# Performance work log

Measured on AMD Instinct MI355X. Metric: run time of the kernel, lower is better.

Reference implementation:

```python
import jax, jax.numpy as jnp
import numpy as np

N_TERMS = 2048  # zonotope error terms (x[0] center + 2047 generators)
N = 4096        # neurons


def setup_inputs() -> dict:
    key = jax.random.key(0)
    x = jax.random.normal(key, (N_TERMS, N), dtype=jnp.float32)
    return {"x": x}


def reference(x):
    n_terms, n = x.shape
    # interval bounds of the zonotope
    abs_sum = jnp.sum(jnp.abs(x[1:]), axis=0)      # [n]
    upper = x[0] + abs_sum
    lower = x[0] - abs_sum

    cross = (lower * upper) < 0                    # neuron straddles 0
    pos = lower >= 0                               # strictly non-negative
    crossf = cross.astype(x.dtype)
    posf = pos.astype(x.dtype)

    # 'auto' lambda init: upper/(upper-lower) on crossing neurons, 1 on positive,
    # NaN (0/0) replaced by 0.5; lambda is set via .data => constant w.r.t. x.
    denom = upper - lower
    safe = denom != 0
    lam = posf + crossf * jnp.where(safe, upper / jnp.where(safe, denom, 1.0), 0.5)
    lam = jax.lax.stop_gradient(lam)

    delta = jnp.maximum(-lam * lower, (1.0 - lam) * upper)  # [n]

    center = (delta * 0.5 + lam * x[0]) * crossf + x[0] * posf
    gens = x[1:] * (lam * crossf + posf)                    # [n_terms-1, n]

    # Parallel stream-compaction: crossing neuron i gets its own new error row
    # at n_terms + (# crossings before i). Padded to worst case n new rows;
    # non-crossing writes land on distinct (row, col) slots with value 0.
    ci = cross.astype(jnp.int32)
    rows = n_terms + jnp.cumsum(ci) - ci               # exclusive prefix sum
    cols = jnp.arange(n)

    out = jnp.zeros((n_terms + n, n), x.dtype)
    out = out.at[0].set(center)
    out = out.at[1:n_terms].set(gens)
    out = out.at[rows, cols].add((delta * 0.5) * crossf)
    return out
```

## Files before the change

kernel.cpp:

```cpp
#include <hip/hip_runtime.h>

#define N_TERMS 2048
#define NCOL 4096
#define NC4 1024
#define NCHUNK 128
#define RPC (N_TERMS / NCHUNK)

typedef float f4_t __attribute__((ext_vector_type(4)));

__global__ void k_pass1(const float* __restrict__ x, float* __restrict__ partial,
                        float* __restrict__ out, int* __restrict__ done_ctr) {
    const int b = blockIdx.x;
    const int t = threadIdx.x;
    if (b < 512) {
        if (b == 0 && t == 0) *done_ctr = 0;
        const int col4 = (b & 3) * 256 + t;
        const int chunk = b >> 2;
        int r0 = chunk * RPC;
        const int r1 = r0 + RPC;
        if (r0 == 0) r0 = 1;
        const f4_t* x4 = (const f4_t*)x;
        f4_t acc = {0.f, 0.f, 0.f, 0.f};
#pragma unroll
        for (int r = r0; r < r1; ++r) {
            f4_t v = x4[(long)r * NC4 + col4];
            acc.x += fabsf(v.x);
            acc.y += fabsf(v.y);
            acc.z += fabsf(v.z);
            acc.w += fabsf(v.w);
        }
        ((f4_t*)partial)[chunk * NC4 + col4] = acc;
    } else {
        const int zb = b - 512;
        f4_t* o4 = (f4_t*)out;
        const long base4 = (long)N_TERMS * NC4 + (long)zb * 2048;
        const f4_t z = {0.f, 0.f, 0.f, 0.f};
#pragma unroll
        for (int i = 0; i < 8; ++i)
            __builtin_nontemporal_store(z, &o4[base4 + i * 256 + t]);
    }
}

__global__ void k_stats(const float* __restrict__ x, const float* __restrict__ partial,
                        float* __restrict__ out, float* __restrict__ scale,
                        float* __restrict__ dhalf, int* __restrict__ crossflag,
                        int* __restrict__ done_ctr) {
    const int t = threadIdx.x;
    const int lane = t & 63;
    const int q = t >> 6;
    const int c = blockIdx.x * 64 + lane;

    float s0 = 0.f, s1 = 0.f, s2 = 0.f, s3 = 0.f;
    const int k0 = q * 32;
#pragma unroll 8
    for (int k = 0; k < 32; k += 4) {
        s0 += partial[(k0 + k + 0) * NCOL + c];
        s1 += partial[(k0 + k + 1) * NCOL + c];
        s2 += partial[(k0 + k + 2) * NCOL + c];
        s3 += partial[(k0 + k + 3) * NCOL + c];
    }
    __shared__ float red[4][64];
    red[q][lane] = (s0 + s1) + (s2 + s3);
    __syncthreads();
    if (q == 0) {
        float s = (red[0][lane] + red[1][lane]) + (red[2][lane] + red[3][lane]);
        float x0 = x[c];
        float u = x0 + s;
        float l = x0 - s;
        bool cross = (l * u) < 0.0f;
        bool pos = (l >= 0.0f);
        float denom = u - l;
        float lam = (pos ? 1.0f : 0.0f) +
                    (cross ? ((denom != 0.0f) ? u / denom : 0.5f) : 0.0f);
        float delta = fmaxf(-lam * l, (1.0f - lam) * u);
        float crossf = cross ? 1.0f : 0.0f;
        float posf = pos ? 1.0f : 0.0f;
        out[c] = (delta * 0.5f + lam * x0) * crossf + x0 * posf;
        scale[c] = lam * crossf + posf;
        dhalf[c] = delta * 0.5f * crossf;
        crossflag[c] = cross ? 1 : 0;
    }

    __threadfence();
    __shared__ int is_last;
    if (t == 0) is_last = (atomicAdd(done_ctr, 1) == (int)gridDim.x - 1);
    __syncthreads();
    if (!is_last) return;
    __threadfence();

    const int T = 256;
    const int PER = NCOL / T;
    __shared__ int tsum[T];
    const int base = t * PER;
    int cf[PER];
    int ex[PER];
    int run = 0;
#pragma unroll
    for (int i = 0; i < PER; ++i) {
        cf[i] = crossflag[base + i];
        ex[i] = run;
        run += cf[i];
    }
    tsum[t] = run;
    __syncthreads();
    for (int off = 1; off < T; off <<= 1) {
        int v = 0;
        if (t >= off) v = tsum[t - off];
        __syncthreads();
        tsum[t] += v;
        __syncthreads();
    }
    const int excl = (t == 0) ? 0 : tsum[t - 1];
#pragma unroll
    for (int i = 0; i < PER; ++i) {
        if (cf[i]) {
            const int c2 = base + i;
            const long row = N_TERMS + excl + ex[i];
            out[row * (long)NCOL + c2] = dhalf[c2];
        }
    }
}

__global__ void k_gens(const float* __restrict__ x, const float* __restrict__ scale,
                       float* __restrict__ out) {
    const int g = blockIdx.x * blockDim.x + threadIdx.x;
    const int col4 = g & 1023;
    const int group = g >> 10;
    const int r0 = group << 2;
    const f4_t* x4 = (const f4_t*)x;
    f4_t* o4 = (f4_t*)out;
    const f4_t sc = ((const f4_t*)scale)[col4];

    if (group == 0) {
#pragma unroll
        for (int r = 1; r < 4; ++r) {
            f4_t v = x4[(long)r * NC4 + col4] * sc;
            __builtin_nontemporal_store(v, &o4[(long)r * NC4 + col4]);
        }
    } else {
#pragma unroll
        for (int i = 0; i < 4; ++i) {
            const int r = r0 + i;
            f4_t v = x4[(long)r * NC4 + col4] * sc;
            __builtin_nontemporal_store(v, &o4[(long)r * NC4 + col4]);
        }
    }
}

extern "C" void kernel_launch(void* const* d_in, const int* in_sizes, int n_in,
                              void* d_out, int out_size, void* d_ws, size_t ws_size,
                              hipStream_t stream) {
    const float* x = (const float*)d_in[0];
    float* out = (float*)d_out;

    float* ws = (float*)d_ws;
    float* partial   = ws;
    float* scale     = partial + NCHUNK * NCOL;
    float* dhalf     = scale + NCOL;
    int*   crossflag = (int*)(dhalf + NCOL);
    int*   done_ctr  = crossflag + NCOL;

    k_pass1<<<2560, 256, 0, stream>>>(x, partial, out, done_ctr);
    k_stats<<<64, 256, 0, stream>>>(x, partial, out, scale, dhalf, crossflag, done_ctr);
    k_gens<<<2048, 256, 0, stream>>>(x, scale, out);
}
```

Measured before the change: 146.5 us.

## Reassign zero-fill and scan across kernels, drop last-block atomic handoff

Moves the zeroing of the padded tail rows from the abs-sum pass into the stats kernel, which now runs 512 extra blocks that each write four times as much, so the zero-fill overlaps the small stats computation. The prefix-scan scatter is taken out of the stats kernel's last-block atomic/threadfence pattern and becomes one extra block in the generator-scaling kernel. This removes the done counter and its fences. The cost is that the serial scan block now runs alongside the large gens kernel instead of alone.

```diff
diff --git a/kernel.cpp b/kernel.cpp
--- a/kernel.cpp
+++ b/kernel.cpp
@@ -8,141 +8,137 @@
 
 typedef float f4_t __attribute__((ext_vector_type(4)));
 
-__global__ void k_pass1(const float* __restrict__ x, float* __restrict__ partial,
-                        float* __restrict__ out, int* __restrict__ done_ctr) {
+__global__ void k_partial_abs(const float* __restrict__ x, float* __restrict__ partial) {
+    int col4 = blockIdx.x * blockDim.x + threadIdx.x;
+    int chunk = blockIdx.y;
+    int r0 = chunk * RPC;
+    int r1 = r0 + RPC;
+    if (r0 == 0) r0 = 1;
+    const f4_t* x4 = (const f4_t*)x;
+    f4_t acc = {0.f, 0.f, 0.f, 0.f};
+#pragma unroll
+    for (int r = r0; r < r1; ++r) {
+        f4_t v = x4[(long)r * NC4 + col4];
+        acc.x += fabsf(v.x);
+        acc.y += fabsf(v.y);
+        acc.z += fabsf(v.z);
+        acc.w += fabsf(v.w);
+    }
+    ((f4_t*)partial)[chunk * NC4 + col4] = acc;
+}
+
+__global__ void k_stats_zero(const float* __restrict__ x, const float* __restrict__ partial,
+                             float* __restrict__ out, float* __restrict__ scale,
+                             float* __restrict__ dhalf, int* __restrict__ crossflag) {
     const int b = blockIdx.x;
     const int t = threadIdx.x;
-    if (b < 512) {
-        if (b == 0 && t == 0) *done_ctr = 0;
-        const int col4 = (b & 3) * 256 + t;
-        const int chunk = b >> 2;
-        int r0 = chunk * RPC;
-        const int r1 = r0 + RPC;
-        if (r0 == 0) r0 = 1;
-        const f4_t* x4 = (const f4_t*)x;
-        f4_t acc = {0.f, 0.f, 0.f, 0.f};
-#pragma unroll
-        for (int r = r0; r < r1; ++r) {
-            f4_t v = x4[(long)r * NC4 + col4];
-            acc.x += fabsf(v.x);
-            acc.y += fabsf(v.y);
-            acc.z += fabsf(v.z);
-            acc.w += fabsf(v.w);
+
+    if (b < 64) {
+        const int lane = t & 63;
+        const int q = t >> 6;
+        const int c = b * 64 + lane;
+
+        float s0 = 0.f, s1 = 0.f, s2 = 0.f, s3 = 0.f;
+        const int k0 = q * 32;
+#pragma unroll 8
+        for (int k = 0; k < 32; k += 4) {
+            s0 += partial[(k0 + k + 0) * NCOL + c];
+            s1 += partial[(k0 + k + 1) * NCOL + c];
+            s2 += partial[(k0 + k + 2) * NCOL + c];
+            s3 += partial[(k0 + k + 3) * NCOL + c];
         }
-        ((f4_t*)partial)[chunk * NC4 + col4] = acc;
+        __shared__ float red[4][64];
+        red[q][lane] = (s0 + s1) + (s2 + s3);
+        __syncthreads();
+        if (q == 0) {
+            float s = (red[0][lane] + red[1][lane]) + (red[2][lane] + red[3][lane]);
+            float x0 = x[c];
+            float u = x0 + s;
+            float l = x0 - s;
+            bool cross = (l * u) < 0.0f;
+            bool pos = (l >= 0.0f);
+            float denom = u - l;
+            float lam = (pos ? 1.0f : 0.0f) +
+                        (cross ? ((denom != 0.0f) ? u / denom : 0.5f) : 0.0f);
+            float delta = fmaxf(-lam * l, (1.0f - lam) * u);
+            float crossf = cross ? 1.0f : 0.0f;
+            float posf = pos ? 1.0f : 0.0f;
+            out[c] = (delta * 0.5f + lam * x0) * crossf + x0 * posf;
+            scale[c] = lam * crossf + posf;
+            dhalf[c] = delta * 0.5f * crossf;
+            crossflag[c] = cross ? 1 : 0;
+        }
     } else {
-        const int zb = b - 512;
+        const int zb = b - 64;
         f4_t* o4 = (f4_t*)out;
-        const long base4 = (long)N_TERMS * NC4 + (long)zb * 2048;
+        const long base4 = (long)N_TERMS * NC4 + (long)zb * 8192;
         const f4_t z = {0.f, 0.f, 0.f, 0.f};
 #pragma unroll
-        for (int i = 0; i < 8; ++i)
+        for (int i = 0; i < 32; ++i)
             __builtin_nontemporal_store(z, &o4[base4 + i * 256 + t]);
     }
 }
 
-__global__ void k_stats(const float* __restrict__ x, const float* __restrict__ partial,
-                        float* __restrict__ out, float* __restrict__ scale,
-                        float* __restrict__ dhalf, int* __restrict__ crossflag,
-                        int* __restrict__ done_ctr) {
+__global__ void k_gens_scatter(const float* __restrict__ x, const float* __restrict__ scale,
+                               const float* __restrict__ dhalf,
+                               const int* __restrict__ crossflag,
+                               float* __restrict__ out) {
+    const int b = blockIdx.x;
     const int t = threadIdx.x;
-    const int lane = t & 63;
-    const int q = t >> 6;
-    const int c = blockIdx.x * 64 + lane;
+    if (b < 2048) {
+        const int g = b * 256 + t;
+        const int col4 = g & 1023;
+        const int group = g >> 10;
+        const int r0 = group << 2;
+        const f4_t* x4 = (const f4_t*)x;
+        f4_t* o4 = (f4_t*)out;
+        const f4_t sc = ((const f4_t*)scale)[col4];
 
-    float s0 = 0.f, s1 = 0.f, s2 = 0.f, s3 = 0.f;
-    const int k0 = q * 32;
-#pragma unroll 8
-    for (int k = 0; k < 32; k += 4) {
-        s0 += partial[(k0 + k + 0) * NCOL + c];
-        s1 += partial[(k0 + k + 1) * NCOL + c];
-        s2 += partial[(k0 + k + 2) * NCOL + c];
-        s3 += partial[(k0 + k + 3) * NCOL + c];
-    }
-    __shared__ float red[4][64];
-    red[q][lane] = (s0 + s1) + (s2 + s3);
-    __syncthreads();
-    if (q == 0) {
-        float s = (red[0][lane] + red[1][lane]) + (red[2][lane] + red[3][lane]);
-        float x0 = x[c];
-        float u = x0 + s;
-        float l = x0 - s;
-        bool cross = (l * u) < 0.0f;
-        bool pos = (l >= 0.0f);
-        float denom = u - l;
-        float lam = (pos ? 1.0f : 0.0f) +
-                    (cross ? ((denom != 0.0f) ? u / denom : 0.5f) : 0.0f);
-        float delta = fmaxf(-lam * l, (1.0f - lam) * u);
-        float crossf = cross ? 1.0f : 0.0f;
-        float posf = pos ? 1.0f : 0.0f;
-        out[c] = (delta * 0.5f + lam * x0) * crossf + x0 * posf;
-        scale[c] = lam * crossf + posf;
-        dhalf[c] = delta * 0.5f * crossf;
-        crossflag[c] = cross ? 1 : 0;
-    }
-
-    __threadfence();
-    __shared__ int is_last;
-    if (t == 0) is_last = (atomicAdd(done_ctr, 1) == (int)gridDim.x - 1);
-    __syncthreads();
-    if (!is_last) return;
-    __threadfence();
-
-    const int T = 256;
-    const int PER = NCOL / T;
-    __shared__ int tsum[T];
-    const int base = t * PER;
-    int cf[PER];
-    int ex[PER];
-    int run = 0;
+        if (group == 0) {
 #pragma unroll
-    for (int i = 0; i < PER; ++i) {
-        cf[i] = crossflag[base + i];
-        ex[i] = run;
-        run += cf[i];
-    }
-    tsum[t] = run;
-    __syncthreads();
-    for (int off = 1; off < T; off <<= 1) {
-        int v = 0;
-        if (t >= off) v = tsum[t - off];
-        __syncthreads();
-        tsum[t] += v;
-        __syncthreads();
-    }
-    const int excl = (t == 0) ? 0 : tsum[t - 1];
+            for (int r = 1; r < 4; ++r) {
+                f4_t v = x4[(long)r * NC4 + col4] * sc;
+                __builtin_nontemporal_store(v, &o4[(long)r * NC4 + col4]);
+            }
+        } else {
 #pragma unroll
-    for (int i = 0; i < PER; ++i) {
-        if (cf[i]) {
-            const int c2 = base + i;
-            const long row = N_TERMS + excl + ex[i];
-            out[row * (long)NCOL + c2] = dhalf[c2];
-        }
-    }
-}
-
-__global__ void k_gens(const float* __restrict__ x, const float* __restrict__ scale,
-                       float* __restrict__ out) {
-    const int g = blockIdx.x * blockDim.x + threadIdx.x;
-    const int col4 = g & 1023;
-    const int group = g >> 10;
-    const int r0 = group << 2;
-    const f4_t* x4 = (const f4_t*)x;
-    f4_t* o4 = (f4_t*)out;
-    const f4_t sc = ((const f4_t*)scale)[col4];
-
-    if (group == 0) {
-#pragma unroll
-        for (int r = 1; r < 4; ++r) {
-            f4_t v = x4[(long)r * NC4 + col4] * sc;
-            __builtin_nontemporal_store(v, &o4[(long)r * NC4 + col4]);
+            for (int i = 0; i < 4; ++i) {
+                const int r = r0 + i;
+                f4_t v = x4[(long)r * NC4 + col4] * sc;
+                __builtin_nontemporal_store(v, &o4[(long)r * NC4 + col4]);
+            }
         }
     } else {
+        const int T = 256;
+        const int PER = NCOL / T;
+        __shared__ int tsum[T];
+        const int base = t * PER;
+        int cf[PER];
+        int ex[PER];
+        int run = 0;
 #pragma unroll
-        for (int i = 0; i < 4; ++i) {
-            const int r = r0 + i;
-            f4_t v = x4[(long)r * NC4 + col4] * sc;
-            __builtin_nontemporal_store(v, &o4[(long)r * NC4 + col4]);
+        for (int i = 0; i < PER; ++i) {
+            cf[i] = crossflag[base + i];
+            ex[i] = run;
+            run += cf[i];
+        }
+        tsum[t] = run;
+        __syncthreads();
+        for (int off = 1; off < T; off <<= 1) {
+            int v = 0;
+            if (t >= off) v = tsum[t - off];
+            __syncthreads();
+            tsum[t] += v;
+            __syncthreads();
+        }
+        const int excl = (t == 0) ? 0 : tsum[t - 1];
+#pragma unroll
+        for (int i = 0; i < PER; ++i) {
+            if (cf[i]) {
+                const int c = base + i;
+                const long row = N_TERMS + excl + ex[i];
+                out[row * (long)NCOL + c] = dhalf[c];
+            }
         }
     }
 }
@@ -158,9 +154,8 @@
     float* scale     = partial + NCHUNK * NCOL;
     float* dhalf     = scale + NCOL;
     int*   crossflag = (int*)(dhalf + NCOL);
-    int*   done_ctr  = crossflag + NCOL;
 
-    k_pass1<<<2560, 256, 0, stream>>>(x, partial, out, done_ctr);
-    k_stats<<<64, 256, 0, stream>>>(x, partial, out, scale, dhalf, crossflag, done_ctr);
-    k_gens<<<2048, 256, 0, stream>>>(x, scale, out);
+    k_partial_abs<<<dim3(NC4 / 256, NCHUNK), 256, 0, stream>>>(x, partial);
+    k_stats_zero<<<576, 256, 0, stream>>>(x, partial, out, scale, dhalf, crossflag);
+    k_gens_scatter<<<2049, 256, 0, stream>>>(x, scale, dhalf, crossflag, out);
 }
```

Measured after the change: 137.1 us. 6.4% less time.
